# Kernel optimization log

Measured on AMD Instinct MI355X. Metric: run time of the kernel, lower is better.

Reference implementation:

```python
import jax, jax.numpy as jnp
import numpy as np

D_MODEL = 1024
NUM_HEADS = 16
D_K = D_MODEL // NUM_HEADS
THETA = 10000.0
BATCH = 2
SEQ = 2048


def _trunc_normal(key, shape, std):
    # approximate trunc_normal init; exact init distribution is irrelevant for correctness
    return jnp.clip(jax.random.normal(key, shape) * std, -3.0 * std, 3.0 * std)


def setup_inputs() -> dict:
    key = jax.random.key(0)
    ks = jax.random.split(key, 6)
    std = np.sqrt(2.0 / (D_MODEL + D_MODEL)).astype(np.float32)
    x = jax.random.normal(ks[0], (BATCH, SEQ, D_MODEL), dtype=jnp.float32)
    token_positions = jnp.tile(jnp.arange(SEQ, dtype=jnp.int32), (BATCH, 1))
    wq = _trunc_normal(ks[1], (D_MODEL, D_MODEL), std)  # (out, in)
    wk = _trunc_normal(ks[2], (D_MODEL, D_MODEL), std)
    wv = _trunc_normal(ks[3], (D_MODEL, D_MODEL), std)
    wo = _trunc_normal(ks[4], (D_MODEL, D_MODEL), std)
    return {"in_features": x, "wq": wq, "wk": wk, "wv": wv, "wo": wo,
            "token_positions": token_positions}


def _apply_rope(x, token_positions):
    # x: (B, H, S, d_k); token_positions: (B, S)
    half = D_K // 2
    inv_freq = 1.0 / (THETA ** (2.0 * jnp.arange(half, dtype=jnp.float32) / D_K))
    ang = token_positions.astype(jnp.float32)[..., None] * inv_freq  # (B, S, half)
    cos = jnp.cos(ang)[:, None, :, :]  # (B, 1, S, half) broadcast over heads
    sin = jnp.sin(ang)[:, None, :, :]
    x_even = x[..., 0::2]
    x_odd = x[..., 1::2]
    rot_even = x_even * cos - x_odd * sin
    rot_odd = x_even * sin + x_odd * cos
    return jnp.stack([rot_even, rot_odd], axis=-1).reshape(x.shape)


def reference(in_features, wq, wk, wv, wo, token_positions):
    B, S, _ = in_features.shape
    # bias-free linear: weight is (out, in)
    q = jnp.einsum('bsi,oi->bso', in_features, wq)
    k = jnp.einsum('bsi,oi->bso', in_features, wk)
    v = jnp.einsum('bsi,oi->bso', in_features, wv)
    # split heads: (B, H, S, d_k)
    def split(t):
        return t.reshape(B, S, NUM_HEADS, D_K).transpose(0, 2, 1, 3)
    qh, kh, vh = split(q), split(k), split(v)
    qh = _apply_rope(qh, token_positions)
    kh = _apply_rope(kh, token_positions)
    scale = 1.0 / jnp.sqrt(jnp.float32(D_K))
    logits = jnp.einsum('bhqd,bhkd->bhqk', qh, kh) * scale  # (B, H, S, S)
    causal = jnp.tril(jnp.ones((S, S), dtype=bool))
    logits = jnp.where(causal, logits, -jnp.inf)
    weights = jax.nn.softmax(logits, axis=-1)
    out = jnp.einsum('bhqk,bhkd->bhqd', weights, vh)  # (B, H, S, d_k)
    out = out.transpose(0, 2, 1, 3).reshape(B, S, D_MODEL)
    return jnp.einsum('bsi,oi->bso', out, wo)
```

## Files before the change

### kernel.cpp

```cpp
#include <hip/hip_runtime.h>
#include <hip/hip_bf16.h>
#include <math.h>

#define D_MODEL 1024
#define NUM_HEADS 16
#define DK 64
#define BATCH 2
#define SEQ 2048
#define NROWS (BATCH * SEQ)

typedef __bf16 bf16x8 __attribute__((ext_vector_type(8)));
typedef __bf16 bf16x4 __attribute__((ext_vector_type(4)));
typedef float f32x4 __attribute__((ext_vector_type(4)));

#define GLOAD_LDS16(g, l)                                          \
  __builtin_amdgcn_global_load_lds(                                \
      (const __attribute__((address_space(1))) void*)(g),          \
      (__attribute__((address_space(3))) void*)(l), 16, 0, 0)

#define LDS_FENCE() asm volatile("s_waitcnt lgkmcnt(0)" ::: "memory")

__global__ void cvt_all_kernel(const float* __restrict__ x,
                               const float* __restrict__ wq,
                               const float* __restrict__ wk,
                               const float* __restrict__ wv,
                               const float* __restrict__ wo,
                               __hip_bfloat16* __restrict__ xb,
                               __hip_bfloat16* __restrict__ wqb,
                               __hip_bfloat16* __restrict__ wkb,
                               __hip_bfloat16* __restrict__ wvb,
                               __hip_bfloat16* __restrict__ wob) {
  int t = blockIdx.x * 256 + threadIdx.x;
  const float* src;
  __hip_bfloat16* dst;
  int off;
  if (t < 1048576) {
    src = x; dst = xb; off = t;
  } else {
    int u = t - 1048576;
    int w = u >> 18;
    off = u & 262143;
    src = (w == 0) ? wq : (w == 1) ? wk : (w == 2) ? wv : wo;
    dst = (w == 0) ? wqb : (w == 1) ? wkb : (w == 2) ? wvb : wob;
  }
  float4 v = reinterpret_cast<const float4*>(src)[off];
  union { __hip_bfloat16 h[4]; uint2 u; } tmp;
  tmp.h[0] = __float2bfloat16(v.x);
  tmp.h[1] = __float2bfloat16(v.y);
  tmp.h[2] = __float2bfloat16(v.z);
  tmp.h[3] = __float2bfloat16(v.w);
  reinterpret_cast<uint2*>(dst)[off] = tmp.u;
}

template <bool OUT_F32>
__global__ __launch_bounds__(256)
void gemm_bt_kernel(const __hip_bfloat16* __restrict__ A,
                    const __hip_bfloat16* __restrict__ W0,
                    const __hip_bfloat16* __restrict__ W1,
                    const __hip_bfloat16* __restrict__ W2,
                    void* __restrict__ O0, void* __restrict__ O1,
                    void* __restrict__ O2) {
  __shared__ __hip_bfloat16 sA[2][128 * 32];
  __shared__ __hip_bfloat16 sB[2][128 * 32];
  const int tid = threadIdx.x;
  const int wave = tid >> 6, lane = tid & 63, quad = lane >> 4, l16 = lane & 15;
  const int wm = (wave >> 1) * 64, wn = (wave & 1) * 64;
  const int bm = blockIdx.x * 128, bn = blockIdx.y * 128;
  const __hip_bfloat16* W = (blockIdx.z == 0) ? W0 : (blockIdx.z == 1) ? W1 : W2;
  void* O = (blockIdx.z == 0) ? O0 : (blockIdx.z == 1) ? O1 : O2;
  const int srow = lane >> 2, scol = (lane & 3) * 8;

#pragma unroll
  for (int c = 0; c < 2; ++c) {
    int ch = wave + c * 4;
    GLOAD_LDS16(&A[(size_t)(bm + ch * 16 + srow) * D_MODEL + scol], &sA[0][ch * 512]);
    GLOAD_LDS16(&W[(size_t)(bn + ch * 16 + srow) * D_MODEL + scol], &sB[0][ch * 512]);
  }

  f32x4 acc[4][4] = {};
  for (int it = 0; it < 32; ++it) {
    __syncthreads();
    if (it + 1 < 32) {
      const int k0 = (it + 1) * 32, nb = (it + 1) & 1;
#pragma unroll
      for (int c = 0; c < 2; ++c) {
        int ch = wave + c * 4;
        GLOAD_LDS16(&A[(size_t)(bm + ch * 16 + srow) * D_MODEL + k0 + scol],
                    &sA[nb][ch * 512]);
        GLOAD_LDS16(&W[(size_t)(bn + ch * 16 + srow) * D_MODEL + k0 + scol],
                    &sB[nb][ch * 512]);
      }
    }
    const int cb = it & 1;
    bf16x8 af[4], bfb[4];
#pragma unroll
    for (int i = 0; i < 4; ++i)
      af[i] = *reinterpret_cast<bf16x8*>(&sA[cb][(wm + i * 16 + l16) * 32 + quad * 8]);
#pragma unroll
    for (int j = 0; j < 4; ++j)
      bfb[j] = *reinterpret_cast<bf16x8*>(&sB[cb][(wn + j * 16 + l16) * 32 + quad * 8]);
#pragma unroll
    for (int i = 0; i < 4; ++i)
#pragma unroll
      for (int j = 0; j < 4; ++j)
        acc[i][j] = __builtin_amdgcn_mfma_f32_16x16x32_bf16(af[i], bfb[j], acc[i][j], 0, 0, 0);
  }

#pragma unroll
  for (int i = 0; i < 4; ++i)
#pragma unroll
    for (int j = 0; j < 4; ++j)
#pragma unroll
      for (int r = 0; r < 4; ++r) {
        int row = bm + wm + i * 16 + quad * 4 + r;
        int col = bn + wn + j * 16 + l16;
        if (OUT_F32)
          reinterpret_cast<float*>(O)[(size_t)row * D_MODEL + col] = acc[i][j][r];
        else
          reinterpret_cast<__hip_bfloat16*>(O)[(size_t)row * D_MODEL + col] =
              __float2bfloat16(acc[i][j][r]);
      }
}

__global__ void rope_kernel(__hip_bfloat16* __restrict__ Q,
                            __hip_bfloat16* __restrict__ K,
                            const int* __restrict__ pos) {
  constexpr float QS = 0.18033688011112042f;
  int t = blockIdx.x * 256 + threadIdx.x;
  int row = t >> 7;
  int c = t & 127;
  int h = c >> 3, co = (c & 7) * 8;
  float ps = (float)pos[row];
  size_t off = (size_t)row * D_MODEL + h * DK + co;
  bf16x8 q = *reinterpret_cast<const bf16x8*>(&Q[off]);
  bf16x8 k = *reinterpret_cast<const bf16x8*>(&K[off]);
#pragma unroll
  for (int j = 0; j < 4; ++j) {
    float p = (float)((co >> 1) + j);
    float ang = ps * exp2f(-p * 0.41524101186091903f);
    float cs = cosf(ang), sn = sinf(ang);
    float qe = (float)q[2 * j], qo = (float)q[2 * j + 1];
    q[2 * j]     = (__bf16)((qe * cs - qo * sn) * QS);
    q[2 * j + 1] = (__bf16)((qe * sn + qo * cs) * QS);
    float ke = (float)k[2 * j], ko = (float)k[2 * j + 1];
    k[2 * j]     = (__bf16)(ke * cs - ko * sn);
    k[2 * j + 1] = (__bf16)(ke * sn + ko * cs);
  }
  *reinterpret_cast<bf16x8*>(&Q[off]) = q;
  *reinterpret_cast<bf16x8*>(&K[off]) = k;
}

__global__ __launch_bounds__(512)
void attn_kernel(const __hip_bfloat16* __restrict__ Q,
                 const __hip_bfloat16* __restrict__ K,
                 const __hip_bfloat16* __restrict__ V,
                 __hip_bfloat16* __restrict__ Ao) {
  constexpr int LS = 66;
  constexpr int LSP = 72;
  __shared__ __hip_bfloat16 sK[2][64 * LS];
  __shared__ __hip_bfloat16 sVt[2][64 * LS];
  __shared__ __hip_bfloat16 sPt[8][16 * LSP];
  __shared__ float sL[8][16];
  const int tid = threadIdx.x;
  const int wave = tid >> 6, lane = tid & 63, quad = lane >> 4, l16 = lane & 15;
  const int idx = blockIdx.x;
  const int qb = 15 - (idx >> 5);
  const int hb = idx & 31;
  const int h = hb & 15, b = hb >> 4;
  const int ho = h * DK;
  const size_t rowbase = (size_t)b * SEQ;
  const int sb = qb * 128 + wave * 16;
  const __hip_bfloat16* Kbase = K + rowbase * D_MODEL + ho;
  const unsigned short* Vu =
      reinterpret_cast<const unsigned short*>(V + rowbase * D_MODEL + ho);

  bf16x8 aq[2];
#pragma unroll
  for (int kk = 0; kk < 2; ++kk)
    aq[kk] = *reinterpret_cast<const bf16x8*>(
        &Q[(rowbase + sb + l16) * D_MODEL + ho + kk * 32 + quad * 8]);

  f32x4 o_acc[4] = {};
  float l_run = 0.f;

  const int krow = tid >> 3, kcol = (tid & 7) * 8;
  const int vd = lane;

  {
    *reinterpret_cast<bf16x8*>(&sK[0][krow * LS + kcol]) =
        *reinterpret_cast<const bf16x8*>(&Kbase[(size_t)krow * D_MODEL + kcol]);
#pragma unroll
    for (int c = 0; c < 4; ++c) {
      int kvp = c * 8 + wave;
      unsigned lo = Vu[(size_t)(2 * kvp) * D_MODEL + vd];
      unsigned hi = Vu[(size_t)(2 * kvp + 1) * D_MODEL + vd];
      *reinterpret_cast<unsigned*>(&sVt[0][vd * LS + 2 * kvp]) = lo | (hi << 16);
    }
  }

  const int nt = 2 * qb + 2;
  for (int t = 0; t < nt; ++t) {
    __syncthreads();
    const int buf = t & 1;
    const bool hn = (t + 1) < nt;
    bf16x8 knext;
    unsigned vw[4];
    if (hn) {
      const int kvn = (t + 1) * 64;
      knext = *reinterpret_cast<const bf16x8*>(
          &Kbase[(size_t)(kvn + krow) * D_MODEL + kcol]);
#pragma unroll
      for (int c = 0; c < 4; ++c) {
        int kvp = c * 8 + wave;
        unsigned lo = Vu[(size_t)(kvn + 2 * kvp) * D_MODEL + vd];
        unsigned hi = Vu[(size_t)(kvn + 2 * kvp + 1) * D_MODEL + vd];
        vw[c] = lo | (hi << 16);
      }
    }

    const int kv0 = t * 64;
    if (kv0 <= sb + 15) {
      f32x4 sv[4] = {};
#pragma unroll
      for (int kk = 0; kk < 2; ++kk)
#pragma unroll
        for (int j = 0; j < 4; ++j) {
          bf16x8 ak = *reinterpret_cast<bf16x8*>(
              &sK[buf][(j * 16 + l16) * LS + kk * 32 + quad * 8]);
          sv[j] = __builtin_amdgcn_mfma_f32_16x16x32_bf16(ak, aq[kk], sv[j], 0, 0, 0);
        }
      if (kv0 + 63 > sb) {
#pragma unroll
        for (int j = 0; j < 4; ++j)
#pragma unroll
          for (int r = 0; r < 4; ++r)
            if (kv0 + j * 16 + quad * 4 + r > sb + l16) sv[j][r] = -INFINITY;
      }
      float ls = 0.f;
#pragma unroll
      for (int j = 0; j < 4; ++j) {
        bf16x4 pk;
#pragma unroll
        for (int r = 0; r < 4; ++r) {
          float p = __builtin_amdgcn_exp2f(sv[j][r]);
          ls += p;
          pk[r] = (__bf16)p;
        }
        *reinterpret_cast<bf16x4*>(&sPt[wave][l16 * LSP + j * 16 + quad * 4]) = pk;
      }
      l_run += ls;
      LDS_FENCE();
#pragma unroll
      for (int kk = 0; kk < 2; ++kk) {
        bf16x8 ap = *reinterpret_cast<bf16x8*>(
            &sPt[wave][l16 * LSP + kk * 32 + quad * 8]);
#pragma unroll
        for (int jd = 0; jd < 4; ++jd) {
          bf16x8 bv = *reinterpret_cast<bf16x8*>(
              &sVt[buf][(jd * 16 + l16) * LS + kk * 32 + quad * 8]);
          o_acc[jd] = __builtin_amdgcn_mfma_f32_16x16x32_bf16(ap, bv, o_acc[jd], 0, 0, 0);
        }
      }
    }

    if (hn) {
      const int nb = buf ^ 1;
      *reinterpret_cast<bf16x8*>(&sK[nb][krow * LS + kcol]) = knext;
#pragma unroll
      for (int c = 0; c < 4; ++c) {
        int kvp = c * 8 + wave;
        *reinterpret_cast<unsigned*>(&sVt[nb][vd * LS + 2 * kvp]) = vw[c];
      }
    }
  }

  float l = l_run;
  l += __shfl_xor(l, 16);
  l += __shfl_xor(l, 32);
  sL[wave][l16] = l;
  LDS_FENCE();
  __hip_bfloat16* Aobase = Ao + (rowbase + sb) * D_MODEL + ho;
#pragma unroll
  for (int r = 0; r < 4; ++r) {
    float linv = 1.0f / sL[wave][quad * 4 + r];
#pragma unroll
    for (int jd = 0; jd < 4; ++jd)
      Aobase[(size_t)(quad * 4 + r) * D_MODEL + jd * 16 + l16] =
          __float2bfloat16(o_acc[jd][r] * linv);
  }
}

extern "C" void kernel_launch(void* const* d_in, const int* in_sizes, int n_in,
                              void* d_out, int out_size, void* d_ws, size_t ws_size,
                              hipStream_t stream) {
  const float* x = (const float*)d_in[0];
  const float* wq = (const float*)d_in[1];
  const float* wk = (const float*)d_in[2];
  const float* wv = (const float*)d_in[3];
  const float* wo = (const float*)d_in[4];
  const int* tpos = (const int*)d_in[5];
  float* out = (float*)d_out;
  char* ws = (char*)d_ws;

  __hip_bfloat16* xb  = (__hip_bfloat16*)(ws);
  __hip_bfloat16* wqb = (__hip_bfloat16*)(ws + (size_t)(8)  * 1048576);
  __hip_bfloat16* wkb = (__hip_bfloat16*)(ws + (size_t)(10) * 1048576);
  __hip_bfloat16* wvb = (__hip_bfloat16*)(ws + (size_t)(12) * 1048576);
  __hip_bfloat16* wob = (__hip_bfloat16*)(ws + (size_t)(14) * 1048576);
  __hip_bfloat16* Qb  = (__hip_bfloat16*)(ws + (size_t)(16) * 1048576);
  __hip_bfloat16* Kb  = (__hip_bfloat16*)(ws + (size_t)(24) * 1048576);
  __hip_bfloat16* Vb  = (__hip_bfloat16*)(ws + (size_t)(32) * 1048576);
  __hip_bfloat16* Aob = xb;

  cvt_all_kernel<<<8192, 256, 0, stream>>>(x, wq, wk, wv, wo,
                                           xb, wqb, wkb, wvb, wob);

  gemm_bt_kernel<false><<<dim3(32, 8, 3), 256, 0, stream>>>(
      xb, wqb, wkb, wvb, Qb, Kb, Vb);

  rope_kernel<<<2048, 256, 0, stream>>>(Qb, Kb, tpos);

  attn_kernel<<<512, 512, 0, stream>>>(Qb, Kb, Vb, Aob);

  gemm_bt_kernel<true><<<dim3(32, 8, 1), 256, 0, stream>>>(
      Aob, wob, wob, wob, out, out, out);
}
```

Before: 218.6 us.

## Halve attention block to 4 waves each handling two query strips, swizzle P LDS

The attention kernel now uses 256 threads, and each wave processes two 16-row query strips paired from opposite ends of the block (wave and 7-wave) to balance causal work. K and V fragments are loaded from LDS once per tile and reused across both strips. The P staging buffer drops its padding and uses an XOR swizzle, and the row-sum normalisation uses shuffles instead of LDS. The QKV weights are packed contiguously so the fused QKV GEMM uses a 2D grid with a single weight pointer. Register pressure rises with doubled accumulators and prefetched fragments, and having fewer threads per block may reduce latency hiding.

```diff
diff --git a/kernel.cpp b/kernel.cpp
--- a/kernel.cpp
+++ b/kernel.cpp
@@ -26,9 +26,7 @@
                                const float* __restrict__ wv,
                                const float* __restrict__ wo,
                                __hip_bfloat16* __restrict__ xb,
-                               __hip_bfloat16* __restrict__ wqb,
-                               __hip_bfloat16* __restrict__ wkb,
-                               __hip_bfloat16* __restrict__ wvb,
+                               __hip_bfloat16* __restrict__ wqkvb,
                                __hip_bfloat16* __restrict__ wob) {
   int t = blockIdx.x * 256 + threadIdx.x;
   const float* src;
@@ -41,7 +39,7 @@
     int w = u >> 18;
     off = u & 262143;
     src = (w == 0) ? wq : (w == 1) ? wk : (w == 2) ? wv : wo;
-    dst = (w == 0) ? wqb : (w == 1) ? wkb : (w == 2) ? wvb : wob;
+    dst = (w < 3) ? (wqkvb + (size_t)w * 1048576) : wob;
   }
   float4 v = reinterpret_cast<const float4*>(src)[off];
   union { __hip_bfloat16 h[4]; uint2 u; } tmp;
@@ -52,12 +50,10 @@
   reinterpret_cast<uint2*>(dst)[off] = tmp.u;
 }
 
-template <bool OUT_F32>
+template <int NSPLIT, bool OUT_F32>
 __global__ __launch_bounds__(256)
 void gemm_bt_kernel(const __hip_bfloat16* __restrict__ A,
-                    const __hip_bfloat16* __restrict__ W0,
-                    const __hip_bfloat16* __restrict__ W1,
-                    const __hip_bfloat16* __restrict__ W2,
+                    const __hip_bfloat16* __restrict__ W,
                     void* __restrict__ O0, void* __restrict__ O1,
                     void* __restrict__ O2) {
   __shared__ __hip_bfloat16 sA[2][128 * 32];
@@ -65,16 +61,25 @@
   const int tid = threadIdx.x;
   const int wave = tid >> 6, lane = tid & 63, quad = lane >> 4, l16 = lane & 15;
   const int wm = (wave >> 1) * 64, wn = (wave & 1) * 64;
-  const int bm = blockIdx.x * 128, bn = blockIdx.y * 128;
-  const __hip_bfloat16* W = (blockIdx.z == 0) ? W0 : (blockIdx.z == 1) ? W1 : W2;
-  void* O = (blockIdx.z == 0) ? O0 : (blockIdx.z == 1) ? O1 : O2;
+  const int bm = blockIdx.x * 128;
+  const int bnG = blockIdx.y * 128;
+  void* O;
+  int ocol;
+  if (NSPLIT == 3) {
+    int which = blockIdx.y >> 3;
+    O = (which == 0) ? O0 : (which == 1) ? O1 : O2;
+    ocol = bnG & 1023;
+  } else {
+    O = O0;
+    ocol = bnG;
+  }
   const int srow = lane >> 2, scol = (lane & 3) * 8;
 
 #pragma unroll
   for (int c = 0; c < 2; ++c) {
     int ch = wave + c * 4;
     GLOAD_LDS16(&A[(size_t)(bm + ch * 16 + srow) * D_MODEL + scol], &sA[0][ch * 512]);
-    GLOAD_LDS16(&W[(size_t)(bn + ch * 16 + srow) * D_MODEL + scol], &sB[0][ch * 512]);
+    GLOAD_LDS16(&W[(size_t)(bnG + ch * 16 + srow) * D_MODEL + scol], &sB[0][ch * 512]);
   }
 
   f32x4 acc[4][4] = {};
@@ -87,7 +92,7 @@
         int ch = wave + c * 4;
         GLOAD_LDS16(&A[(size_t)(bm + ch * 16 + srow) * D_MODEL + k0 + scol],
                     &sA[nb][ch * 512]);
-        GLOAD_LDS16(&W[(size_t)(bn + ch * 16 + srow) * D_MODEL + k0 + scol],
+        GLOAD_LDS16(&W[(size_t)(bnG + ch * 16 + srow) * D_MODEL + k0 + scol],
                     &sB[nb][ch * 512]);
       }
     }
@@ -113,7 +118,7 @@
 #pragma unroll
       for (int r = 0; r < 4; ++r) {
         int row = bm + wm + i * 16 + quad * 4 + r;
-        int col = bn + wn + j * 16 + l16;
+        int col = ocol + wn + j * 16 + l16;
         if (OUT_F32)
           reinterpret_cast<float*>(O)[(size_t)row * D_MODEL + col] = acc[i][j][r];
         else
@@ -150,17 +155,15 @@
   *reinterpret_cast<bf16x8*>(&K[off]) = k;
 }
 
-__global__ __launch_bounds__(512)
+__global__ __launch_bounds__(256)
 void attn_kernel(const __hip_bfloat16* __restrict__ Q,
                  const __hip_bfloat16* __restrict__ K,
                  const __hip_bfloat16* __restrict__ V,
                  __hip_bfloat16* __restrict__ Ao) {
   constexpr int LS = 66;
-  constexpr int LSP = 72;
   __shared__ __hip_bfloat16 sK[2][64 * LS];
   __shared__ __hip_bfloat16 sVt[2][64 * LS];
-  __shared__ __hip_bfloat16 sPt[8][16 * LSP];
-  __shared__ float sL[8][16];
+  __shared__ __hip_bfloat16 sPt[4][16 * 64];
   const int tid = threadIdx.x;
   const int wave = tid >> 6, lane = tid & 63, quad = lane >> 4, l16 = lane & 15;
   const int idx = blockIdx.x;
@@ -169,29 +172,33 @@
   const int h = hb & 15, b = hb >> 4;
   const int ho = h * DK;
   const size_t rowbase = (size_t)b * SEQ;
-  const int sb = qb * 128 + wave * 16;
+  const int sbs[2] = {qb * 128 + wave * 16, qb * 128 + (7 - wave) * 16};
   const __hip_bfloat16* Kbase = K + rowbase * D_MODEL + ho;
   const unsigned short* Vu =
       reinterpret_cast<const unsigned short*>(V + rowbase * D_MODEL + ho);
 
-  bf16x8 aq[2];
-#pragma unroll
-  for (int kk = 0; kk < 2; ++kk)
-    aq[kk] = *reinterpret_cast<const bf16x8*>(
-        &Q[(rowbase + sb + l16) * D_MODEL + ho + kk * 32 + quad * 8]);
-
-  f32x4 o_acc[4] = {};
-  float l_run = 0.f;
-
-  const int krow = tid >> 3, kcol = (tid & 7) * 8;
+  bf16x8 aq[2][2];
+#pragma unroll
+  for (int s = 0; s < 2; ++s)
+#pragma unroll
+    for (int kk = 0; kk < 2; ++kk)
+      aq[s][kk] = *reinterpret_cast<const bf16x8*>(
+          &Q[(rowbase + sbs[s] + l16) * D_MODEL + ho + kk * 32 + quad * 8]);
+
+  f32x4 o_acc[2][4] = {};
+  float l_run[2] = {0.f, 0.f};
+
+  const int krow = tid >> 2, kc = (tid & 3) * 16;
   const int vd = lane;
 
   {
-    *reinterpret_cast<bf16x8*>(&sK[0][krow * LS + kcol]) =
-        *reinterpret_cast<const bf16x8*>(&Kbase[(size_t)krow * D_MODEL + kcol]);
-#pragma unroll
-    for (int c = 0; c < 4; ++c) {
-      int kvp = c * 8 + wave;
+    *reinterpret_cast<bf16x8*>(&sK[0][krow * LS + kc]) =
+        *reinterpret_cast<const bf16x8*>(&Kbase[(size_t)krow * D_MODEL + kc]);
+    *reinterpret_cast<bf16x8*>(&sK[0][krow * LS + kc + 8]) =
+        *reinterpret_cast<const bf16x8*>(&Kbase[(size_t)krow * D_MODEL + kc + 8]);
+#pragma unroll
+    for (int i = 0; i < 8; ++i) {
+      int kvp = wave * 8 + i;
       unsigned lo = Vu[(size_t)(2 * kvp) * D_MODEL + vd];
       unsigned hi = Vu[(size_t)(2 * kvp + 1) * D_MODEL + vd];
       *reinterpret_cast<unsigned*>(&sVt[0][vd * LS + 2 * kvp]) = lo | (hi << 16);
@@ -203,32 +210,46 @@
     __syncthreads();
     const int buf = t & 1;
     const bool hn = (t + 1) < nt;
-    bf16x8 knext;
-    unsigned vw[4];
+    bf16x8 kn0, kn1;
+    unsigned vw[8];
     if (hn) {
       const int kvn = (t + 1) * 64;
-      knext = *reinterpret_cast<const bf16x8*>(
-          &Kbase[(size_t)(kvn + krow) * D_MODEL + kcol]);
-#pragma unroll
-      for (int c = 0; c < 4; ++c) {
-        int kvp = c * 8 + wave;
+      kn0 = *reinterpret_cast<const bf16x8*>(
+          &Kbase[(size_t)(kvn + krow) * D_MODEL + kc]);
+      kn1 = *reinterpret_cast<const bf16x8*>(
+          &Kbase[(size_t)(kvn + krow) * D_MODEL + kc + 8]);
+#pragma unroll
+      for (int i = 0; i < 8; ++i) {
+        int kvp = wave * 8 + i;
         unsigned lo = Vu[(size_t)(kvn + 2 * kvp) * D_MODEL + vd];
         unsigned hi = Vu[(size_t)(kvn + 2 * kvp + 1) * D_MODEL + vd];
-        vw[c] = lo | (hi << 16);
+        vw[i] = lo | (hi << 16);
       }
     }
 
     const int kv0 = t * 64;
-    if (kv0 <= sb + 15) {
+    bf16x8 ak[2][4], bv[2][4];
+#pragma unroll
+    for (int kk = 0; kk < 2; ++kk)
+#pragma unroll
+      for (int j = 0; j < 4; ++j) {
+        ak[kk][j] = *reinterpret_cast<bf16x8*>(
+            &sK[buf][(j * 16 + l16) * LS + kk * 32 + quad * 8]);
+        bv[kk][j] = *reinterpret_cast<bf16x8*>(
+            &sVt[buf][(j * 16 + l16) * LS + kk * 32 + quad * 8]);
+      }
+
+#pragma unroll
+    for (int s = 0; s < 2; ++s) {
+      const int sb = sbs[s];
+      if (kv0 > sb + 15) continue;
       f32x4 sv[4] = {};
 #pragma unroll
       for (int kk = 0; kk < 2; ++kk)
 #pragma unroll
-        for (int j = 0; j < 4; ++j) {
-          bf16x8 ak = *reinterpret_cast<bf16x8*>(
-              &sK[buf][(j * 16 + l16) * LS + kk * 32 + quad * 8]);
-          sv[j] = __builtin_amdgcn_mfma_f32_16x16x32_bf16(ak, aq[kk], sv[j], 0, 0, 0);
-        }
+        for (int j = 0; j < 4; ++j)
+          sv[j] = __builtin_amdgcn_mfma_f32_16x16x32_bf16(ak[kk][j], aq[s][kk],
+                                                          sv[j], 0, 0, 0);
       if (kv0 + 63 > sb) {
 #pragma unroll
         for (int j = 0; j < 4; ++j)
@@ -246,47 +267,49 @@
           ls += p;
           pk[r] = (__bf16)p;
         }
-        *reinterpret_cast<bf16x4*>(&sPt[wave][l16 * LSP + j * 16 + quad * 4]) = pk;
-      }
-      l_run += ls;
+        int wgr = (2 * j + (quad >> 1)) ^ (l16 & 7);
+        *reinterpret_cast<bf16x4*>(
+            &sPt[wave][l16 * 64 + wgr * 8 + (quad & 1) * 4]) = pk;
+      }
+      l_run[s] += ls;
       LDS_FENCE();
 #pragma unroll
       for (int kk = 0; kk < 2; ++kk) {
-        bf16x8 ap = *reinterpret_cast<bf16x8*>(
-            &sPt[wave][l16 * LSP + kk * 32 + quad * 8]);
-#pragma unroll
-        for (int jd = 0; jd < 4; ++jd) {
-          bf16x8 bv = *reinterpret_cast<bf16x8*>(
-              &sVt[buf][(jd * 16 + l16) * LS + kk * 32 + quad * 8]);
-          o_acc[jd] = __builtin_amdgcn_mfma_f32_16x16x32_bf16(ap, bv, o_acc[jd], 0, 0, 0);
-        }
+        int rgr = (4 * kk + quad) ^ (l16 & 7);
+        bf16x8 ap = *reinterpret_cast<bf16x8*>(&sPt[wave][l16 * 64 + rgr * 8]);
+#pragma unroll
+        for (int jd = 0; jd < 4; ++jd)
+          o_acc[s][jd] = __builtin_amdgcn_mfma_f32_16x16x32_bf16(
+              ap, bv[kk][jd], o_acc[s][jd], 0, 0, 0);
       }
     }
 
     if (hn) {
       const int nb = buf ^ 1;
-      *reinterpret_cast<bf16x8*>(&sK[nb][krow * LS + kcol]) = knext;
-#pragma unroll
-      for (int c = 0; c < 4; ++c) {
-        int kvp = c * 8 + wave;
-        *reinterpret_cast<unsigned*>(&sVt[nb][vd * LS + 2 * kvp]) = vw[c];
-      }
-    }
-  }
-
-  float l = l_run;
-  l += __shfl_xor(l, 16);
-  l += __shfl_xor(l, 32);
-  sL[wave][l16] = l;
-  LDS_FENCE();
-  __hip_bfloat16* Aobase = Ao + (rowbase + sb) * D_MODEL + ho;
-#pragma unroll
-  for (int r = 0; r < 4; ++r) {
-    float linv = 1.0f / sL[wave][quad * 4 + r];
-#pragma unroll
-    for (int jd = 0; jd < 4; ++jd)
-      Aobase[(size_t)(quad * 4 + r) * D_MODEL + jd * 16 + l16] =
-          __float2bfloat16(o_acc[jd][r] * linv);
+      *reinterpret_cast<bf16x8*>(&sK[nb][krow * LS + kc]) = kn0;
+      *reinterpret_cast<bf16x8*>(&sK[nb][krow * LS + kc + 8]) = kn1;
+#pragma unroll
+      for (int i = 0; i < 8; ++i) {
+        int kvp = wave * 8 + i;
+        *reinterpret_cast<unsigned*>(&sVt[nb][vd * LS + 2 * kvp]) = vw[i];
+      }
+    }
+  }
+
+#pragma unroll
+  for (int s = 0; s < 2; ++s) {
+    float l = l_run[s];
+    l += __shfl_xor(l, 16);
+    l += __shfl_xor(l, 32);
+    __hip_bfloat16* Aobase = Ao + (rowbase + sbs[s]) * D_MODEL + ho;
+#pragma unroll
+    for (int r = 0; r < 4; ++r) {
+      float linv = 1.0f / __shfl(l, quad * 4 + r);
+#pragma unroll
+      for (int jd = 0; jd < 4; ++jd)
+        Aobase[(size_t)(quad * 4 + r) * D_MODEL + jd * 16 + l16] =
+            __float2bfloat16(o_acc[s][jd][r] * linv);
+    }
   }
 }
 
@@ -302,26 +325,23 @@
   float* out = (float*)d_out;
   char* ws = (char*)d_ws;
 
-  __hip_bfloat16* xb  = (__hip_bfloat16*)(ws);
-  __hip_bfloat16* wqb = (__hip_bfloat16*)(ws + (size_t)(8)  * 1048576);
-  __hip_bfloat16* wkb = (__hip_bfloat16*)(ws + (size_t)(10) * 1048576);
-  __hip_bfloat16* wvb = (__hip_bfloat16*)(ws + (size_t)(12) * 1048576);
-  __hip_bfloat16* wob = (__hip_bfloat16*)(ws + (size_t)(14) * 1048576);
-  __hip_bfloat16* Qb  = (__hip_bfloat16*)(ws + (size_t)(16) * 1048576);
-  __hip_bfloat16* Kb  = (__hip_bfloat16*)(ws + (size_t)(24) * 1048576);
-  __hip_bfloat16* Vb  = (__hip_bfloat16*)(ws + (size_t)(32) * 1048576);
-  __hip_bfloat16* Aob = xb;
-
-  cvt_all_kernel<<<8192, 256, 0, stream>>>(x, wq, wk, wv, wo,
-                                           xb, wqb, wkb, wvb, wob);
-
-  gemm_bt_kernel<false><<<dim3(32, 8, 3), 256, 0, stream>>>(
-      xb, wqb, wkb, wvb, Qb, Kb, Vb);
+  __hip_bfloat16* xb    = (__hip_bfloat16*)(ws);
+  __hip_bfloat16* wqkvb = (__hip_bfloat16*)(ws + (size_t)(8)  * 1048576);
+  __hip_bfloat16* wob   = (__hip_bfloat16*)(ws + (size_t)(14) * 1048576);
+  __hip_bfloat16* Qb    = (__hip_bfloat16*)(ws + (size_t)(16) * 1048576);
+  __hip_bfloat16* Kb    = (__hip_bfloat16*)(ws + (size_t)(24) * 1048576);
+  __hip_bfloat16* Vb    = (__hip_bfloat16*)(ws + (size_t)(32) * 1048576);
+  __hip_bfloat16* Aob   = xb;
+
+  cvt_all_kernel<<<8192, 256, 0, stream>>>(x, wq, wk, wv, wo, xb, wqkvb, wob);
+
+  gemm_bt_kernel<3, false><<<dim3(32, 24), 256, 0, stream>>>(
+      xb, wqkvb, Qb, Kb, Vb);
 
   rope_kernel<<<2048, 256, 0, stream>>>(Qb, Kb, tpos);
 
-  attn_kernel<<<512, 512, 0, stream>>>(Qb, Kb, Vb, Aob);
-
-  gemm_bt_kernel<true><<<dim3(32, 8, 1), 256, 0, stream>>>(
-      Aob, wob, wob, wob, out, out, out);
-}
+  attn_kernel<<<512, 256, 0, stream>>>(Qb, Kb, Vb, Aob);
+
+  gemm_bt_kernel<1, true><<<dim3(32, 8), 256, 0, stream>>>(
+      Aob, wob, out, out, out);
+}
```

New measurement: 217.7 us. About the same (-0.4%).
